# Kernel tuning notes

Measured on AMD Instinct MI355X. Metric: run time of the kernel, lower is better.

The kernel has to match this reference:

```python
import jax, jax.numpy as jnp
import numpy as np

DIM = 768
HEADS = 12

def setup_inputs() -> dict:
    key = jax.random.key(0)
    ks = jax.random.split(key, 5)
    x = jax.random.normal(ks[0], (8, 1024, DIM), dtype=jnp.float32)
    s = 1.0 / np.sqrt(DIM)
    W_qkv = jax.random.normal(ks[1], (DIM, 3 * DIM), dtype=jnp.float32) * s
    b_qkv = jax.random.normal(ks[2], (3 * DIM,), dtype=jnp.float32) * 0.01
    W_proj = jax.random.normal(ks[3], (DIM, DIM), dtype=jnp.float32) * s
    b_proj = jax.random.normal(ks[4], (DIM,), dtype=jnp.float32) * 0.01
    return {"x": x, "W_qkv": W_qkv, "b_qkv": b_qkv, "W_proj": W_proj, "b_proj": b_proj}

def reference(x, W_qkv, b_qkv, W_proj, b_proj):
    B, T, D = x.shape
    H = HEADS
    hd = D // H
    scale = hd ** -0.5
    qkv = x @ W_qkv + b_qkv                      # [B,T,3D]
    qkv = qkv.reshape(B, T, 3, H, hd)
    q, k, v = jnp.moveaxis(qkv, 2, 0)            # each [B,T,H,hd]
    q = jnp.transpose(q, (0, 2, 1, 3))           # [B,H,T,hd]
    k = jnp.transpose(k, (0, 2, 1, 3))
    v = jnp.transpose(v, (0, 2, 1, 3))
    attn = jnp.einsum('bhqd,bhkd->bhqk', q, k) * scale
    attn = jax.nn.softmax(attn, axis=-1)
    y = jnp.einsum('bhqk,bhkd->bhqd', attn, v)   # [B,H,T,hd]
    y = jnp.transpose(y, (0, 2, 1, 3)).reshape(B, T, D)
    return y @ W_proj + b_proj
```

## Files before the change

### kernel.cpp

```cpp
#include <hip/hip_runtime.h>

typedef unsigned short u16;
typedef __attribute__((ext_vector_type(8))) short short8;
typedef __attribute__((ext_vector_type(4))) short short4v;
typedef __attribute__((ext_vector_type(2))) int int2v;
typedef __attribute__((ext_vector_type(4))) float f32x4;

#define DIM   768
#define HEADS 12
#define HD    64
#define BATCH 8
#define SEQ   1024
#define MTOK  (BATCH*SEQ)
#define NQKV  (3*DIM)
#define KPAD  72
#define EPAD  66
#define PSZ   ((size_t)BATCH*HEADS*SEQ*HD)
#define SCQ   0.1803368801f

__device__ __forceinline__ u16 f2bf(float f) {
  unsigned x = __float_as_uint(f);
  x += 0x7fffu + ((x >> 16) & 1u);
  return (u16)(x >> 16);
}

__device__ __forceinline__ void gload16(const u16* g, u16* l) {
  __builtin_amdgcn_global_load_lds(
      (const __attribute__((address_space(1))) unsigned int*)g,
      (__attribute__((address_space(3))) unsigned int*)l, 16, 0, 0);
}

#define XBLK 6144
#define QTBLK 1728
__global__ void cvt_all_k(const float* __restrict__ x,
                          const float* __restrict__ Wqkv,
                          const float* __restrict__ Wproj,
                          u16* __restrict__ xb, u16* __restrict__ wqkvt,
                          u16* __restrict__ wprojt) {
  __shared__ u16 tile[32][33];
  const int blk = blockIdx.x;
  if (blk < XBLK) {
    const int i = blk * 256 + threadIdx.x;
    float4 f = ((const float4*)x)[i];
    short4v o;
    o.x = (short)f2bf(f.x); o.y = (short)f2bf(f.y);
    o.z = (short)f2bf(f.z); o.w = (short)f2bf(f.w);
    ((short4v*)xb)[i] = o;
    return;
  }
  const float* in; u16* out; int K, N, n0, k0;
  if (blk < XBLK + QTBLK) {
    const int t = blk - XBLK;
    in = Wqkv; out = wqkvt; K = DIM; N = NQKV;
    n0 = (t % (NQKV / 32)) * 32; k0 = (t / (NQKV / 32)) * 32;
  } else {
    const int t = blk - XBLK - QTBLK;
    in = Wproj; out = wprojt; K = DIM; N = DIM;
    n0 = (t % (DIM / 32)) * 32; k0 = (t / (DIM / 32)) * 32;
  }
  const int tx = threadIdx.x & 31, ty = threadIdx.x >> 5;
  #pragma unroll
  for (int i = 0; i < 32; i += 8)
    tile[ty + i][tx] = f2bf(in[(size_t)(k0 + ty + i) * N + n0 + tx]);
  __syncthreads();
  #pragma unroll
  for (int i = 0; i < 32; i += 8)
    out[(size_t)(n0 + ty + i) * K + k0 + tx] = tile[tx][ty + i];
}

__global__ __launch_bounds__(256)
void gemm_qkv(const u16* __restrict__ A, const u16* __restrict__ Bt,
              const float* __restrict__ bias, u16* __restrict__ qkv) {
  __shared__ __align__(16) u16 smem[8 * 128 * 32];
  const int w = threadIdx.x >> 6, lane = threadIdx.x & 63;
  const int l15 = lane & 15, quad = lane >> 4;
  const int b_ = blockIdx.x;
  const int xcd = b_ & 7, j = b_ >> 3;
  const int m0 = ((j & 7) * 8 + xcd) * 128;
  const int n0 = (j >> 3) * 128;
  const int wm = (w >> 1) * 64, wn = (w & 1) * 64;

  f32x4 acc[4][4] = {};

  const int ar = threadIdx.x >> 2, ak = (threadIdx.x & 3) * 8;
  const u16* ga = A  + (size_t)(m0 + ar) * DIM + ak;
  const u16* gb = Bt + (size_t)(n0 + ar) * DIM + ak;
  const int lo = threadIdx.x * 8;

  auto qstage = [&](int c, int k0) {
    u16* base = smem + c * 16384;
    #pragma unroll
    for (int t = 0; t < 2; ++t) {
      gload16(ga + (size_t)t * 64 * DIM + k0,      base + lo + t * 2048);
      gload16(ga + (size_t)t * 64 * DIM + k0 + 32, base + 4096  + lo + t * 2048);
      gload16(gb + (size_t)t * 64 * DIM + k0,      base + 8192  + lo + t * 2048);
      gload16(gb + (size_t)t * 64 * DIM + k0 + 32, base + 12288 + lo + t * 2048);
    }
  };

  qstage(0, 0);
  __syncthreads();

  #pragma unroll
  for (int it = 0; it < 12; ++it) {
    const int cur = it & 1;
    if (it < 11) qstage(cur ^ 1, (it + 1) * 64);
    const u16* hb = smem + cur * 16384;
    #pragma unroll
    for (int kh = 0; kh < 2; ++kh) {
      const u16* lAh = hb + kh * 4096;
      const u16* lBh = hb + 8192 + kh * 4096;
      short8 af[4], bfr[4];
      #pragma unroll
      for (int mt = 0; mt < 4; ++mt)
        af[mt] = *(const short8*)&lAh[(wm + mt * 16 + l15) * 32 + quad * 8];
      #pragma unroll
      for (int nt = 0; nt < 4; ++nt)
        bfr[nt] = *(const short8*)&lBh[(wn + nt * 16 + l15) * 32 + quad * 8];
      #pragma unroll
      for (int mt = 0; mt < 4; ++mt)
        #pragma unroll
        for (int nt = 0; nt < 4; ++nt)
          acc[mt][nt] = __builtin_amdgcn_mfma_f32_16x16x32_bf16(af[mt], bfr[nt], acc[mt][nt], 0, 0, 0);
    }
    __syncthreads();
  }

  const int bb = m0 >> 10;
  const int tb0 = (m0 & 1023) + wm;
  const int nh = n0 + wn;
  const int part = nh / DIM, idx = nh - part * DIM;
  const int h = idx >> 6;

  float bnl[4];
  #pragma unroll
  for (int nt = 0; nt < 4; ++nt) bnl[nt] = bias[nh + nt * 16 + l15];

  if (part < 2) {
    u16* dstbase = qkv + part * PSZ + ((size_t)(bb * HEADS + h) * SEQ + tb0) * HD;
    const float qsc = (part == 0) ? SCQ : 1.0f;
    const int erow = lane >> 3, ec8 = (lane & 7) * 8;
    #pragma unroll
    for (int mt = 0; mt < 4; ++mt) {
      u16* ep = smem + w * (16 * EPAD) + (mt & 1) * (4 * 16 * EPAD);
      #pragma unroll
      for (int nt = 0; nt < 4; ++nt)
        #pragma unroll
        for (int r = 0; r < 4; ++r)
          ep[(quad * 4 + r) * EPAD + nt * 16 + l15] = f2bf((acc[mt][nt][r] + bnl[nt]) * qsc);
      #pragma unroll
      for (int j2 = 0; j2 < 2; ++j2) {
        const int trow = j2 * 8 + erow;
        short8 vrow = *(const short8*)&ep[trow * EPAD + ec8];
        *(short8*)(dstbase + (size_t)(mt * 16 + trow) * HD + ec8) = vrow;
      }
    }
  } else {
    u16* vrow0 = qkv + 2 * PSZ + (size_t)(bb * HEADS + h) * HD * SEQ;
    #pragma unroll
    for (int nt = 0; nt < 4; ++nt) {
      const int d = nt * 16 + l15;
      u16* trow = vrow0 + (size_t)d * SEQ + tb0 + quad * 4;
      #pragma unroll
      for (int mt = 0; mt < 4; ++mt) {
        short4v pv;
        pv.x = (short)f2bf(acc[mt][nt][0] + bnl[nt]);
        pv.y = (short)f2bf(acc[mt][nt][1] + bnl[nt]);
        pv.z = (short)f2bf(acc[mt][nt][2] + bnl[nt]);
        pv.w = (short)f2bf(acc[mt][nt][3] + bnl[nt]);
        *(short4v*)(trow + mt * 16) = pv;
      }
    }
  }
}

__global__ __launch_bounds__(256)
void gemm_proj(const u16* __restrict__ A, const u16* __restrict__ Bt,
               const float* __restrict__ bias, float* __restrict__ outF) {
  __shared__ __align__(16) u16 smem[2 * 12288];
  const int w = threadIdx.x >> 6, lane = threadIdx.x & 63;
  const int l15 = lane & 15, quad = lane >> 4;
  const int b_ = blockIdx.x;
  const int xcd = b_ & 7, j = b_ >> 3;
  const int m0 = ((j & 7) * 8 + xcd) * 128;
  const int n0 = (j >> 3) * 64;
  const int wm = w * 32;

  f32x4 acc[2][4] = {};

  const int ar = threadIdx.x >> 2, ak = (threadIdx.x & 3) * 8;
  const u16* ga = A  + (size_t)(m0 + ar) * DIM + ak;
  const u16* gb = Bt + (size_t)(n0 + ar) * DIM + ak;
  const int lo = threadIdx.x * 8;

  auto pstage = [&](int c, int k0) {
    u16* base = smem + c * 12288;
    #pragma unroll
    for (int t = 0; t < 2; ++t) {
      gload16(ga + (size_t)t * 64 * DIM + k0,      base + lo + t * 2048);
      gload16(ga + (size_t)t * 64 * DIM + k0 + 32, base + 4096 + lo + t * 2048);
    }
    gload16(gb + k0,      base + 8192  + lo);
    gload16(gb + k0 + 32, base + 10240 + lo);
  };

  pstage(0, 0);
  __syncthreads();

  #pragma unroll
  for (int it = 0; it < 12; ++it) {
    const int cur = it & 1;
    if (it < 11) pstage(cur ^ 1, (it + 1) * 64);
    const u16* hb = smem + cur * 12288;
    #pragma unroll
    for (int kh = 0; kh < 2; ++kh) {
      const u16* lAh = hb + kh * 4096;
      const u16* lBh = hb + 8192 + kh * 2048;
      short8 af[2], bfr[4];
      #pragma unroll
      for (int mt = 0; mt < 2; ++mt)
        af[mt] = *(const short8*)&lAh[(wm + mt * 16 + l15) * 32 + quad * 8];
      #pragma unroll
      for (int nt = 0; nt < 4; ++nt)
        bfr[nt] = *(const short8*)&lBh[(nt * 16 + l15) * 32 + quad * 8];
      #pragma unroll
      for (int mt = 0; mt < 2; ++mt)
        #pragma unroll
        for (int nt = 0; nt < 4; ++nt)
          acc[mt][nt] = __builtin_amdgcn_mfma_f32_16x16x32_bf16(af[mt], bfr[nt], acc[mt][nt], 0, 0, 0);
    }
    __syncthreads();
  }

  #pragma unroll
  for (int nt = 0; nt < 4; ++nt) {
    const int n = n0 + nt * 16 + l15;
    const float bn = bias[n];
    #pragma unroll
    for (int mt = 0; mt < 2; ++mt)
      #pragma unroll
      for (int r = 0; r < 4; ++r) {
        const int m = m0 + wm + mt * 16 + quad * 4 + r;
        outF[(size_t)m * DIM + n] = acc[mt][nt][r] + bn;
      }
  }
}

__global__ __launch_bounds__(512, 6)
void attn_k(const u16* __restrict__ qb, const u16* __restrict__ kb,
            const u16* __restrict__ vtb, u16* __restrict__ yb) {
  const int bh = blockIdx.x, qt = blockIdx.y;
  const int tid = threadIdx.x;
  const int w = tid >> 6, lane = tid & 63;
  const int l15 = lane & 15, quad = lane >> 4;

  __shared__ __align__(16) u16 lK[64 * KPAD];
  __shared__ __align__(16) u16 lV[64 * KPAD];
  __shared__ __align__(16) u16 lP[8][16 * KPAD];

  const u16* qrow = qb + ((size_t)bh * SEQ + qt * 128 + w * 16 + l15) * HD;
  short8 aq0 = *(const short8*)(qrow + quad * 8);
  short8 aq1 = *(const short8*)(qrow + 32 + quad * 8);

  f32x4 o[4] = {};
  f32x4 sum = {};

  const u16* kcbase = kb + (size_t)bh * SEQ * HD;
  const u16* vbase  = vtb + (size_t)bh * HD * SEQ;
  u16* lPw = &lP[w][0];

  const int sofs = (tid >> 3) * KPAD + (tid & 7) * 8;
  const u16* kg = kcbase + tid * 8;
  const u16* vg = vbase + (size_t)(tid >> 3) * SEQ + (tid & 7) * 8;

  short8 pk = *(const short8*)kg;
  short8 pv = *(const short8*)vg;

  short8 ones;
  #pragma unroll
  for (int i = 0; i < 8; ++i) ones[i] = (short)0x3f80;

  for (int kc = 0; kc < 16; ++kc) {
    *(short8*)&lK[sofs] = pk;
    *(short8*)&lV[sofs] = pv;
    __syncthreads();

    const int kn = (kc < 15) ? kc + 1 : 15;
    pk = *(const short8*)(kg + (size_t)kn * 64 * HD);
    pv = *(const short8*)(vg + kn * 64);

    f32x4 st[4];
    __builtin_amdgcn_s_setprio(1);
    #pragma unroll
    for (int nt = 0; nt < 4; ++nt) {
      short8 ak0 = *(const short8*)&lK[(nt * 16 + l15) * KPAD + quad * 8];
      short8 ak1 = *(const short8*)&lK[(nt * 16 + l15) * KPAD + 32 + quad * 8];
      f32x4 z = {};
      z      = __builtin_amdgcn_mfma_f32_16x16x32_bf16(ak0, aq0, z, 0, 0, 0);
      st[nt] = __builtin_amdgcn_mfma_f32_16x16x32_bf16(ak1, aq1, st[nt] = z, 0, 0, 0);
    }
    __builtin_amdgcn_s_setprio(0);

    #pragma unroll
    for (int nt = 0; nt < 4; ++nt) {
      float p0 = __builtin_amdgcn_exp2f(st[nt][0]);
      float p1 = __builtin_amdgcn_exp2f(st[nt][1]);
      float p2 = __builtin_amdgcn_exp2f(st[nt][2]);
      float p3 = __builtin_amdgcn_exp2f(st[nt][3]);
      int2v pkk;
      pkk.x = (int)__builtin_amdgcn_perm(__float_as_uint(p1), __float_as_uint(p0), 0x07060302u);
      pkk.y = (int)__builtin_amdgcn_perm(__float_as_uint(p3), __float_as_uint(p2), 0x07060302u);
      *(int2v*)&lPw[l15 * KPAD + nt * 16 + quad * 4] = pkk;
    }
    const short8 ap0 = *(const short8*)&lPw[l15 * KPAD + quad * 8];
    const short8 ap1 = *(const short8*)&lPw[l15 * KPAD + 32 + quad * 8];

    __builtin_amdgcn_s_setprio(1);
    #pragma unroll
    for (int nt = 0; nt < 4; ++nt) {
      short8 bv0 = *(const short8*)&lV[(nt * 16 + l15) * KPAD + quad * 8];
      short8 bv1 = *(const short8*)&lV[(nt * 16 + l15) * KPAD + 32 + quad * 8];
      o[nt] = __builtin_amdgcn_mfma_f32_16x16x32_bf16(ap0, bv0, o[nt], 0, 0, 0);
      o[nt] = __builtin_amdgcn_mfma_f32_16x16x32_bf16(ap1, bv1, o[nt], 0, 0, 0);
    }
    sum = __builtin_amdgcn_mfma_f32_16x16x32_bf16(ap0, ones, sum, 0, 0, 0);
    sum = __builtin_amdgcn_mfma_f32_16x16x32_bf16(ap1, ones, sum, 0, 0, 0);
    __builtin_amdgcn_s_setprio(0);
    __syncthreads();
  }

  const int b = bh / HEADS, h = bh % HEADS;
  #pragma unroll
  for (int r = 0; r < 4; ++r) {
    const float inv = 1.0f / sum[r];
    #pragma unroll
    for (int nt = 0; nt < 4; ++nt)
      lPw[(quad * 4 + r) * KPAD + nt * 16 + l15] = f2bf(o[nt][r] * inv);
  }

  u16* dst = yb + ((size_t)b * SEQ + qt * 128 + w * 16) * DIM + h * HD;
  const int erow = lane >> 3, ec8 = (lane & 7) * 8;
  #pragma unroll
  for (int j = 0; j < 2; ++j) {
    const int trow = j * 8 + erow;
    short8 vrow = *(const short8*)&lPw[trow * KPAD + ec8];
    *(short8*)(dst + (size_t)trow * DIM + ec8) = vrow;
  }
}

extern "C" void kernel_launch(void* const* d_in, const int* in_sizes, int n_in,
                              void* d_out, int out_size, void* d_ws, size_t ws_size,
                              hipStream_t stream) {
  const float* x     = (const float*)d_in[0];
  const float* Wqkv  = (const float*)d_in[1];
  const float* bqkv  = (const float*)d_in[2];
  const float* Wproj = (const float*)d_in[3];
  const float* bproj = (const float*)d_in[4];
  float* out = (float*)d_out;

  u16* xb     = (u16*)d_ws;
  u16* wqkvt  = xb + (size_t)MTOK * DIM;
  u16* wprojt = wqkvt + (size_t)NQKV * DIM;
  u16* qkv_b  = wprojt + (size_t)DIM * DIM;
  u16* y_b    = qkv_b + 3 * PSZ;

  cvt_all_k<<<XBLK + QTBLK + (DIM / 32) * (DIM / 32), 256, 0, stream>>>(
      x, Wqkv, Wproj, xb, wqkvt, wprojt);

  gemm_qkv<<<1152, 256, 0, stream>>>(xb, wqkvt, bqkv, qkv_b);

  attn_k<<<dim3(BATCH * HEADS, SEQ / 128), 512, 0, stream>>>(
      qkv_b, qkv_b + PSZ, qkv_b + 2 * PSZ, y_b);

  gemm_proj<<<768, 256, 0, stream>>>(y_b, wprojt, bproj, out);
}
```

Baseline: 180.4 us.

## Split attention key dimension across wave pairs with LDS reduction of partial outputs

Each wave now handles 32 query rows against half of every 64-key chunk, instead of 16 query rows against the whole chunk. K fragments are reused across two query groups, and each wave reads only half of the V columns. The two halves' partial O and row sums are then combined through shared memory before normalization and store. LDS row padding changes from 72 to 66 elements, which leaves 16-byte vector accesses misaligned. The shared buffer also grows, which may reduce blocks per CU.

```diff
diff --git a/kernel.cpp b/kernel.cpp
--- a/kernel.cpp
+++ b/kernel.cpp
@@ -13,7 +13,7 @@
 #define SEQ   1024
 #define MTOK  (BATCH*SEQ)
 #define NQKV  (3*DIM)
-#define KPAD  72
+#define KP    66
 #define EPAD  66
 #define PSZ   ((size_t)BATCH*HEADS*SEQ*HD)
 #define SCQ   0.1803368801f
@@ -253,25 +253,34 @@
   const int tid = threadIdx.x;
   const int w = tid >> 6, lane = tid & 63;
   const int l15 = lane & 15, quad = lane >> 4;
-
-  __shared__ __align__(16) u16 lK[64 * KPAD];
-  __shared__ __align__(16) u16 lV[64 * KPAD];
-  __shared__ __align__(16) u16 lP[8][16 * KPAD];
-
-  const u16* qrow = qb + ((size_t)bh * SEQ + qt * 128 + w * 16 + l15) * HD;
-  short8 aq0 = *(const short8*)(qrow + quad * 8);
-  short8 aq1 = *(const short8*)(qrow + 32 + quad * 8);
-
-  f32x4 o[4] = {};
-  f32x4 sum = {};
+  const int rg = w & 3;
+  const int kh = w >> 2;
+  const int nt0 = kh * 2;
+
+  __shared__ __align__(16) u16 smem[25344];
+  u16* lK  = smem;
+  u16* lV  = smem + 4224;
+  u16* lPq = smem + 8448 + rg * 2112;
+  u16* stg = smem + 16896 + rg * 2112;
+
+  const u16* qrow = qb + ((size_t)bh * SEQ + qt * 128 + rg * 32 + l15) * HD;
+  short8 aq[2][2];
+  #pragma unroll
+  for (int qg = 0; qg < 2; ++qg) {
+    aq[qg][0] = *(const short8*)(qrow + (size_t)qg * 16 * HD + quad * 8);
+    aq[qg][1] = *(const short8*)(qrow + (size_t)qg * 16 * HD + 32 + quad * 8);
+  }
+
+  f32x4 o[2][4] = {};
+  f32x4 sum[2] = {};
 
   const u16* kcbase = kb + (size_t)bh * SEQ * HD;
   const u16* vbase  = vtb + (size_t)bh * HD * SEQ;
-  u16* lPw = &lP[w][0];
-
-  const int sofs = (tid >> 3) * KPAD + (tid & 7) * 8;
+
+  const int srow = tid >> 3, scol = tid & 7;
+  const int sofs = srow * KP + scol * 8;
   const u16* kg = kcbase + tid * 8;
-  const u16* vg = vbase + (size_t)(tid >> 3) * SEQ + (tid & 7) * 8;
+  const u16* vg = vbase + (size_t)srow * SEQ + scol * 8;
 
   short8 pk = *(const short8*)kg;
   short8 pv = *(const short8*)vg;
@@ -289,62 +298,94 @@
     pk = *(const short8*)(kg + (size_t)kn * 64 * HD);
     pv = *(const short8*)(vg + kn * 64);
 
-    f32x4 st[4];
-    __builtin_amdgcn_s_setprio(1);
-    #pragma unroll
-    for (int nt = 0; nt < 4; ++nt) {
-      short8 ak0 = *(const short8*)&lK[(nt * 16 + l15) * KPAD + quad * 8];
-      short8 ak1 = *(const short8*)&lK[(nt * 16 + l15) * KPAD + 32 + quad * 8];
-      f32x4 z = {};
-      z      = __builtin_amdgcn_mfma_f32_16x16x32_bf16(ak0, aq0, z, 0, 0, 0);
-      st[nt] = __builtin_amdgcn_mfma_f32_16x16x32_bf16(ak1, aq1, st[nt] = z, 0, 0, 0);
-    }
-    __builtin_amdgcn_s_setprio(0);
-
-    #pragma unroll
-    for (int nt = 0; nt < 4; ++nt) {
-      float p0 = __builtin_amdgcn_exp2f(st[nt][0]);
-      float p1 = __builtin_amdgcn_exp2f(st[nt][1]);
-      float p2 = __builtin_amdgcn_exp2f(st[nt][2]);
-      float p3 = __builtin_amdgcn_exp2f(st[nt][3]);
-      int2v pkk;
-      pkk.x = (int)__builtin_amdgcn_perm(__float_as_uint(p1), __float_as_uint(p0), 0x07060302u);
-      pkk.y = (int)__builtin_amdgcn_perm(__float_as_uint(p3), __float_as_uint(p2), 0x07060302u);
-      *(int2v*)&lPw[l15 * KPAD + nt * 16 + quad * 4] = pkk;
-    }
-    const short8 ap0 = *(const short8*)&lPw[l15 * KPAD + quad * 8];
-    const short8 ap1 = *(const short8*)&lPw[l15 * KPAD + 32 + quad * 8];
-
-    __builtin_amdgcn_s_setprio(1);
-    #pragma unroll
-    for (int nt = 0; nt < 4; ++nt) {
-      short8 bv0 = *(const short8*)&lV[(nt * 16 + l15) * KPAD + quad * 8];
-      short8 bv1 = *(const short8*)&lV[(nt * 16 + l15) * KPAD + 32 + quad * 8];
-      o[nt] = __builtin_amdgcn_mfma_f32_16x16x32_bf16(ap0, bv0, o[nt], 0, 0, 0);
-      o[nt] = __builtin_amdgcn_mfma_f32_16x16x32_bf16(ap1, bv1, o[nt], 0, 0, 0);
-    }
-    sum = __builtin_amdgcn_mfma_f32_16x16x32_bf16(ap0, ones, sum, 0, 0, 0);
-    sum = __builtin_amdgcn_mfma_f32_16x16x32_bf16(ap1, ones, sum, 0, 0, 0);
-    __builtin_amdgcn_s_setprio(0);
+    short8 akf[2][2];
+    #pragma unroll
+    for (int i = 0; i < 2; ++i) {
+      const int key = (nt0 + i) * 16 + l15;
+      akf[i][0] = *(const short8*)&lK[key * KP + quad * 8];
+      akf[i][1] = *(const short8*)&lK[key * KP + 32 + quad * 8];
+    }
+
+    #pragma unroll
+    for (int qg = 0; qg < 2; ++qg) {
+      f32x4 s0 = {}, s1 = {};
+      __builtin_amdgcn_s_setprio(1);
+      s0 = __builtin_amdgcn_mfma_f32_16x16x32_bf16(akf[0][0], aq[qg][0], s0, 0, 0, 0);
+      s0 = __builtin_amdgcn_mfma_f32_16x16x32_bf16(akf[0][1], aq[qg][1], s0, 0, 0, 0);
+      s1 = __builtin_amdgcn_mfma_f32_16x16x32_bf16(akf[1][0], aq[qg][0], s1, 0, 0, 0);
+      s1 = __builtin_amdgcn_mfma_f32_16x16x32_bf16(akf[1][1], aq[qg][1], s1, 0, 0, 0);
+      __builtin_amdgcn_s_setprio(0);
+      #pragma unroll
+      for (int i = 0; i < 2; ++i) {
+        const f32x4 s = i ? s1 : s0;
+        float p0 = __builtin_amdgcn_exp2f(s[0]);
+        float p1 = __builtin_amdgcn_exp2f(s[1]);
+        float p2 = __builtin_amdgcn_exp2f(s[2]);
+        float p3 = __builtin_amdgcn_exp2f(s[3]);
+        int2v pkk;
+        pkk.x = (int)__builtin_amdgcn_perm(__float_as_uint(p1), __float_as_uint(p0), 0x07060302u);
+        pkk.y = (int)__builtin_amdgcn_perm(__float_as_uint(p3), __float_as_uint(p2), 0x07060302u);
+        *(int2v*)&lPq[(qg * 16 + l15) * KP + (nt0 + i) * 16 + quad * 4] = pkk;
+      }
+    }
+
+    short8 bv[4];
+    #pragma unroll
+    for (int ntd = 0; ntd < 4; ++ntd)
+      bv[ntd] = *(const short8*)&lV[(ntd * 16 + l15) * KP + kh * 32 + quad * 8];
+
+    #pragma unroll
+    for (int qg = 0; qg < 2; ++qg) {
+      const short8 ap = *(const short8*)&lPq[(qg * 16 + l15) * KP + kh * 32 + quad * 8];
+      __builtin_amdgcn_s_setprio(1);
+      #pragma unroll
+      for (int ntd = 0; ntd < 4; ++ntd)
+        o[qg][ntd] = __builtin_amdgcn_mfma_f32_16x16x32_bf16(ap, bv[ntd], o[qg][ntd], 0, 0, 0);
+      sum[qg] = __builtin_amdgcn_mfma_f32_16x16x32_bf16(ap, ones, sum[qg], 0, 0, 0);
+      __builtin_amdgcn_s_setprio(0);
+    }
     __syncthreads();
   }
 
-  const int b = bh / HEADS, h = bh % HEADS;
-  #pragma unroll
-  for (int r = 0; r < 4; ++r) {
-    const float inv = 1.0f / sum[r];
-    #pragma unroll
-    for (int nt = 0; nt < 4; ++nt)
-      lPw[(quad * 4 + r) * KPAD + nt * 16 + l15] = f2bf(o[nt][r] * inv);
-  }
-
-  u16* dst = yb + ((size_t)b * SEQ + qt * 128 + w * 16) * DIM + h * HD;
-  const int erow = lane >> 3, ec8 = (lane & 7) * 8;
-  #pragma unroll
-  for (int j = 0; j < 2; ++j) {
-    const int trow = j * 8 + erow;
-    short8 vrow = *(const short8*)&lPw[trow * KPAD + ec8];
-    *(short8*)(dst + (size_t)trow * DIM + ec8) = vrow;
+  float* fo = (float*)smem;
+  if (kh == 1) {
+    #pragma unroll
+    for (int qg = 0; qg < 2; ++qg)
+      #pragma unroll
+      for (int r = 0; r < 4; ++r) {
+        const int row = rg * 32 + qg * 16 + quad * 4 + r;
+        #pragma unroll
+        for (int ntd = 0; ntd < 4; ++ntd)
+          fo[row * 66 + ntd * 16 + l15] = o[qg][ntd][r];
+        if (l15 == 0) fo[row * 66 + 64] = sum[qg][r];
+      }
+  }
+  __syncthreads();
+
+  if (kh == 0) {
+    const int b = bh / HEADS, h = bh % HEADS;
+    #pragma unroll
+    for (int qg = 0; qg < 2; ++qg)
+      #pragma unroll
+      for (int r = 0; r < 4; ++r) {
+        const int lrow = qg * 16 + quad * 4 + r;
+        const int row = rg * 32 + lrow;
+        const float s = sum[qg][r] + fo[row * 66 + 64];
+        const float inv = 1.0f / s;
+        #pragma unroll
+        for (int ntd = 0; ntd < 4; ++ntd) {
+          const float v = (o[qg][ntd][r] + fo[row * 66 + ntd * 16 + l15]) * inv;
+          stg[lrow * KP + ntd * 16 + l15] = f2bf(v);
+        }
+      }
+    u16* dst = yb + ((size_t)b * SEQ + qt * 128 + rg * 32) * DIM + h * HD;
+    const int erow = lane >> 3, ec8 = (lane & 7) * 8;
+    #pragma unroll
+    for (int j = 0; j < 4; ++j) {
+      const int trow = j * 8 + erow;
+      short8 vrow = *(const short8*)&stg[trow * KP + ec8];
+      *(short8*)(dst + (size_t)trow * DIM + ec8) = vrow;
+    }
   }
 }
 
```

New measurement: 329.9 us. +82.9%, slower.
